# Kernel optimization log

Hardware: AMD Instinct MI355X
Metric: run time of the kernel (lower is better)

The kernel has to match this reference:

```python
import jax, jax.numpy as jnp
import numpy as np

N = 100000
E = 1600000
IN_CH = 128
HID = 64      # hidden_channels, heads=1 -> out_ch per head = 64
OUT = 40      # final classes, heads=1, concat=False -> mean over 1 head
SLOPE = 0.2   # leaky relu slope


def setup_inputs() -> dict:
    key = jax.random.key(0)
    k = jax.random.split(key, 6)
    x = jax.random.normal(k[0], (N, IN_CH), dtype=jnp.float32)
    edge_index = jax.random.randint(k[1], (2, E), 0, N, dtype=jnp.int32)
    # xavier-ish scales
    W0 = jax.random.normal(k[2], (HID, IN_CH), dtype=jnp.float32) * (2.0 / (HID + IN_CH)) ** 0.5
    att0 = jax.random.normal(k[3], (1, 1, 2 * HID), dtype=jnp.float32) * 0.1
    W1 = jax.random.normal(k[4], (OUT, HID), dtype=jnp.float32) * (2.0 / (OUT + HID)) ** 0.5
    att1 = jax.random.normal(k[5], (1, 1, 2 * OUT), dtype=jnp.float32) * 0.1
    return {"x": x, "edge_index": edge_index, "W0": W0, "att0": att0, "W1": W1, "att1": att1}


def _gat_conv(h_in, src, dst, W, att, out_ch, concat):
    # h_in: (N, in_ch) -> h: (N, 1, out_ch)   (heads = 1)
    h = (h_in @ W.T).reshape(N, 1, out_ch)
    x_i = h[dst]                                   # (Etot, 1, out_ch) target feats
    x_j = h[src]                                   # (Etot, 1, out_ch) source feats
    logits = jnp.sum(jnp.concatenate([x_i, x_j], axis=-1) * att, axis=-1)  # (Etot, 1)
    logits = jax.nn.leaky_relu(logits, negative_slope=SLOPE)
    # segment softmax over destination node
    m = jax.ops.segment_max(logits, dst, num_segments=N)
    e = jnp.exp(logits - m[dst])
    s = jax.ops.segment_sum(e, dst, num_segments=N)
    alpha = e / s[dst]                             # (Etot, 1)
    out = jax.ops.segment_sum(x_j * alpha[..., None], dst, num_segments=N)  # (N, 1, out_ch)
    return out.reshape(N, out_ch) if concat else out.mean(axis=1)


def reference(x, edge_index, W0, att0, W1, att1):
    # add_self_loops (applied inside each GATConv with the same node count)
    loops = jnp.arange(N, dtype=edge_index.dtype)
    ei = jnp.concatenate([edge_index, jnp.stack([loops, loops])], axis=1)
    src, dst = ei[0], ei[1]  # PyG source_to_target: x_j = x[src], x_i = x[dst]
    h = _gat_conv(x, src, dst, W0, att0, HID, concat=True)
    h = jax.nn.relu(h)  # dropout inactive in eval mode
    h = _gat_conv(h, src, dst, W1, att1, OUT, concat=False)
    return jax.nn.log_softmax(h, axis=1)
```

## Files before the change

### kernel.cpp

```cpp
#include <hip/hip_runtime.h>
#include <math.h>

#define NNODES 100000
#define NEDGES 1600000
#define ETOT   (NEDGES + NNODES)

#define BSZ   128
#define KBUCK ((NNODES + BSZ - 1) / BSZ)
#define CAP   2816
#define NSUB  8
#define CAPS  768
#define CPAD  16

#define GEMMB 1563
#define EPT   4
#define BUCKB ((ETOT + 1024 - 1) / 1024)
#define GGRP  ((GEMMB + 7) / 8)
#define BGRP  ((BUCKB + 7) / 8)

__device__ __forceinline__ int xcc_id() {
    int x;
    asm volatile("s_getreg_b32 %0, hwreg(HW_REG_XCC_ID)" : "=s"(x));
    return x & (NSUB - 1);
}

__device__ __forceinline__ unsigned short f2bf(float f) {
    unsigned u = __float_as_uint(f);
    return (unsigned short)((u + 0x7FFFu + ((u >> 16) & 1u)) >> 16);
}

__global__ void zero_cnt(int* __restrict__ cnt) {
    int i = blockIdx.x * blockDim.x + threadIdx.x;
    if (i < KBUCK * NSUB * CPAD) cnt[i] = 0;
}

__device__ __forceinline__ void bucket_body(int bb, const int* __restrict__ ei,
                                            int* __restrict__ cnt,
                                            unsigned int* __restrict__ stage) {
    const int t = threadIdx.x;
    const int xg = xcc_id();
#pragma unroll
    for (int r = 0; r < EPT; ++r) {
        int e = bb * 1024 + r * 256 + t;
        if (e < ETOT) {
            int src, dst;
            if (e < NEDGES) { src = ei[e]; dst = ei[NEDGES + e]; }
            else            { src = dst = e - NEDGES; }
            int sb = (dst >> 7) * NSUB + xg;
            int pos = atomicAdd(&cnt[sb * CPAD], 1);
            if (pos < CAPS)
                stage[(size_t)sb * CAPS + pos] =
                    ((unsigned)(dst & 127) << 24) | (unsigned)src;
        }
    }
}

__device__ __forceinline__ void gemm0_body(int gb, const float* __restrict__ x,
                                           const float* __restrict__ W,
                                           const float* __restrict__ att,
                                           unsigned short* __restrict__ h0b,
                                           float* __restrict__ ai,
                                           float* __restrict__ aj) {
    __shared__ float Wt[64 * 68];
    const int tid = threadIdx.x;
    const int nb = gb * 64;

    const int lane = tid & 63;
    const int w    = tid >> 6;
    const int ocg  = lane & 15;
    const int ng   = lane >> 4;
    const int nodeLocal = w * 16 + ng * 4;

    const float* xp[4];
#pragma unroll
    for (int j = 0; j < 4; ++j) {
        int node = nb + nodeLocal + j;
        xp[j] = x + (size_t)(node < NNODES ? node : NNODES - 1) * 128;
    }

    float4 acc[4];
#pragma unroll
    for (int j = 0; j < 4; ++j) acc[j] = make_float4(0.f, 0.f, 0.f, 0.f);

#pragma unroll
    for (int h = 0; h < 2; ++h) {
        if (h) __syncthreads();
        for (int i = tid; i < 64 * 64; i += 256) {
            int oc = i >> 6, k = i & 63;
            Wt[k * 68 + oc] = W[oc * 128 + h * 64 + k];
        }
        __syncthreads();

#pragma unroll 4
        for (int k4 = 0; k4 < 16; ++k4) {
            const int kb = k4 * 4;
            float4 wv0 = *(const float4*)&Wt[(kb + 0) * 68 + ocg * 4];
            float4 wv1 = *(const float4*)&Wt[(kb + 1) * 68 + ocg * 4];
            float4 wv2 = *(const float4*)&Wt[(kb + 2) * 68 + ocg * 4];
            float4 wv3 = *(const float4*)&Wt[(kb + 3) * 68 + ocg * 4];
#pragma unroll
            for (int j = 0; j < 4; ++j) {
                float4 xv = *(const float4*)(xp[j] + h * 64 + kb);
                acc[j].x += xv.x * wv0.x + xv.y * wv1.x + xv.z * wv2.x + xv.w * wv3.x;
                acc[j].y += xv.x * wv0.y + xv.y * wv1.y + xv.z * wv2.y + xv.w * wv3.y;
                acc[j].z += xv.x * wv0.z + xv.y * wv1.z + xv.z * wv2.z + xv.w * wv3.z;
                acc[j].w += xv.x * wv0.w + xv.y * wv1.w + xv.z * wv2.w + xv.w * wv3.w;
            }
        }
    }

    const int ocb = ocg * 4;
    float ati[4], atj[4];
#pragma unroll
    for (int i = 0; i < 4; ++i) {
        ati[i] = att[ocb + i];
        atj[i] = att[64 + ocb + i];
    }

#pragma unroll
    for (int j = 0; j < 4; ++j) {
        int nodeG = nb + nodeLocal + j;
        float pai = acc[j].x * ati[0] + acc[j].y * ati[1] + acc[j].z * ati[2] + acc[j].w * ati[3];
        float paj = acc[j].x * atj[0] + acc[j].y * atj[1] + acc[j].z * atj[2] + acc[j].w * atj[3];
#pragma unroll
        for (int off = 1; off < 16; off <<= 1) {
            pai += __shfl_xor(pai, off, 64);
            paj += __shfl_xor(paj, off, 64);
        }
        if (nodeG < NNODES) {
            unsigned p0 = ((unsigned)f2bf(acc[j].y) << 16) | f2bf(acc[j].x);
            unsigned p1 = ((unsigned)f2bf(acc[j].w) << 16) | f2bf(acc[j].z);
            *(uint2*)&h0b[(size_t)nodeG * 64 + ocb] = make_uint2(p0, p1);
            if (ocg == 0) { ai[nodeG] = pai; aj[nodeG] = paj; }
        }
    }
}

__global__ __launch_bounds__(256) void fusedA(
        const int* __restrict__ ei, int* __restrict__ cnt,
        unsigned int* __restrict__ stage,
        const float* __restrict__ x, const float* __restrict__ W0,
        const float* __restrict__ att0,
        unsigned short* __restrict__ h0b, float* __restrict__ ai0,
        float* __restrict__ aj0) {
    const int bid = blockIdx.x;
    const int grp = bid >> 3, sub = bid & 7;
    if ((grp & 1) && (grp >> 1) < GGRP) {
        int g = (grp >> 1) * 8 + sub;
        if (g < GEMMB) gemm0_body(g, x, W0, att0, h0b, ai0, aj0);
    } else {
        int bg = grp - min(GGRP, (grp + 1) >> 1);
        int bb = bg * 8 + sub;
        if (bb < BUCKB) bucket_body(bb, ei, cnt, stage);
    }
}

__global__ void bucket_scan(const int* __restrict__ cnt, int* __restrict__ bstart) {
    __shared__ int wsum[16];
    const int t = threadIdx.x;
    int x = 0;
    if (t < KBUCK) {
#pragma unroll
        for (int s = 0; s < NSUB; ++s) x += min(cnt[(t * NSUB + s) * CPAD], CAPS);
    }
    int lane = t & 63, w = t >> 6;
    int inc = x;
#pragma unroll
    for (int off = 1; off < 64; off <<= 1) {
        int u = __shfl_up(inc, off, 64);
        if (lane >= off) inc += u;
    }
    if (lane == 63) wsum[w] = inc;
    __syncthreads();
    if (t == 0) {
        int s = 0;
#pragma unroll
        for (int j = 0; j < 16; ++j) { int y = wsum[j]; wsum[j] = s; s += y; }
    }
    __syncthreads();
    int excl = inc - x + wsum[w];
    if (t < KBUCK) bstart[t] = excl;
    if (t == KBUCK) bstart[KBUCK] = excl;
}

__global__ __launch_bounds__(256) void bucket_scatter(
        const int* __restrict__ cnt, const int* __restrict__ bstart,
        const unsigned int* __restrict__ stage, int* __restrict__ rowstart,
        int* __restrict__ csr_src) {
    __shared__ unsigned int ent[CAP];
    __shared__ int hist[BSZ];
    __shared__ int scnt[NSUB];
    __shared__ int soff[NSUB + 1];
    __shared__ int wtot;
    const int b = blockIdx.x, t = threadIdx.x;
    const int n0 = b * BSZ;
    const int base = bstart[b];

    if (t < BSZ) hist[t] = 0;
    if (t < NSUB) scnt[t] = min(cnt[(b * NSUB + t) * CPAD], CAPS);
    __syncthreads();
    if (t == 0) {
        int s = 0;
#pragma unroll
        for (int x = 0; x < NSUB; ++x) { soff[x] = s; s += scnt[x]; }
        soff[NSUB] = s;
    }
    __syncthreads();

#pragma unroll
    for (int x = 0; x < NSUB; ++x) {
        const int cx = scnt[x];
        const int ox = soff[x];
        const unsigned int* sp = stage + (size_t)(b * NSUB + x) * CAPS;
        for (int i = t; i < cx; i += 256) {
            unsigned int v = sp[i];
            ent[ox + i] = v;
            atomicAdd(&hist[v >> 24], 1);
        }
    }
    __syncthreads();
    const int c = soff[NSUB];

    int lane = t & 63, w = t >> 6;
    int v = (t < BSZ) ? hist[t] : 0;
    int inc = v;
#pragma unroll
    for (int off = 1; off < 64; off <<= 1) {
        int u = __shfl_up(inc, off, 64);
        if (lane >= off) inc += u;
    }
    if (t == 63) wtot = inc;
    __syncthreads();
    int excl = inc - v + ((w == 1) ? wtot : 0);
    if (t < BSZ) {
        int node = n0 + t;
        if (node <= NNODES) rowstart[node] = base + excl;
    }
    __syncthreads();
    if (t < BSZ) hist[t] = excl;
    __syncthreads();
    for (int i = t; i < c; i += 256) {
        unsigned int e = ent[i];
        int pos = atomicAdd(&hist[e >> 24], 1);
        csr_src[base + pos] = (int)(e & 0xFFFFFFu);
    }
}

__global__ __launch_bounds__(256) void agg_gemm1(
        const int* __restrict__ rowstart, const int* __restrict__ csr_src,
        const float* __restrict__ aj,
        const float* __restrict__ ai, const unsigned short* __restrict__ h0b,
        const float* __restrict__ W1, const float* __restrict__ att1,
        unsigned short* __restrict__ h1b, float* __restrict__ ai1,
        float* __restrict__ aj1) {
    __shared__ float  W1L[64 * 68];
    __shared__ int2   escr[4][64];
    __shared__ float  rowbuf[4][64];

    const int tid = threadIdx.x;
    for (int i = tid; i < 64 * 64; i += 256) {
        int oc = i >> 6, k = i & 63;
        W1L[oc * 68 + k] = (oc < 40) ? W1[oc * 64 + k] : 0.0f;
    }
    __syncthreads();

    const int lane = tid & 63;
    const int wid  = tid >> 6;
    const int n = blockIdx.x * 4 + wid;
    if (n >= NNODES) return;

    const int start = rowstart[n];
    const int end   = rowstart[n + 1];
    const float ain = ai[n];

    const int cg = lane & 7;
    const int sg = lane >> 3;
    float4 accA = make_float4(0.f, 0.f, 0.f, 0.f);
    float4 accB = make_float4(0.f, 0.f, 0.f, 0.f);
    float  esum = 0.0f;

    for (int c = start; c < end; c += 64) {
        int rem = end - c;
        int cnt = (rem < 64) ? rem : 64;
        int s = 0; float e = 0.0f;
        if (lane < cnt) {
            s = csr_src[c + lane];
            float t = ain + aj[s];
            t = (t > 0.0f) ? t : 0.2f * t;
            e = __expf(t);
        }
        escr[wid][lane] = make_int2(s, __float_as_int(e));
        esum += e;
        for (int j0 = 0; j0 < cnt; j0 += 8) {
            int j = j0 + sg;
            if (j < cnt) {
                int2 v = escr[wid][j];
                float a = __int_as_float(v.y);
                uint4 hv = *(const uint4*)&h0b[(size_t)v.x * 64 + cg * 8];
                float c0 = __uint_as_float(hv.x << 16);
                float c1 = __uint_as_float(hv.x & 0xFFFF0000u);
                float c2 = __uint_as_float(hv.y << 16);
                float c3 = __uint_as_float(hv.y & 0xFFFF0000u);
                float c4 = __uint_as_float(hv.z << 16);
                float c5 = __uint_as_float(hv.z & 0xFFFF0000u);
                float c6 = __uint_as_float(hv.w << 16);
                float c7 = __uint_as_float(hv.w & 0xFFFF0000u);
                accA.x = fmaf(a, c0, accA.x);
                accA.y = fmaf(a, c1, accA.y);
                accA.z = fmaf(a, c2, accA.z);
                accA.w = fmaf(a, c3, accA.w);
                accB.x = fmaf(a, c4, accB.x);
                accB.y = fmaf(a, c5, accB.y);
                accB.z = fmaf(a, c6, accB.z);
                accB.w = fmaf(a, c7, accB.w);
            }
        }
    }
#pragma unroll
    for (int off = 32; off > 0; off >>= 1) esum += __shfl_xor(esum, off, 64);
    const float inv = 1.0f / esum;
#pragma unroll
    for (int off = 8; off < 64; off <<= 1) {
        accA.x += __shfl_xor(accA.x, off, 64);
        accA.y += __shfl_xor(accA.y, off, 64);
        accA.z += __shfl_xor(accA.z, off, 64);
        accA.w += __shfl_xor(accA.w, off, 64);
        accB.x += __shfl_xor(accB.x, off, 64);
        accB.y += __shfl_xor(accB.y, off, 64);
        accB.z += __shfl_xor(accB.z, off, 64);
        accB.w += __shfl_xor(accB.w, off, 64);
    }
    if (sg == 0) {
        float4 rA, rB;
        rA.x = fmaxf(accA.x * inv, 0.0f);
        rA.y = fmaxf(accA.y * inv, 0.0f);
        rA.z = fmaxf(accA.z * inv, 0.0f);
        rA.w = fmaxf(accA.w * inv, 0.0f);
        rB.x = fmaxf(accB.x * inv, 0.0f);
        rB.y = fmaxf(accB.y * inv, 0.0f);
        rB.z = fmaxf(accB.z * inv, 0.0f);
        rB.w = fmaxf(accB.w * inv, 0.0f);
        *(float4*)&rowbuf[wid][cg * 8]     = rA;
        *(float4*)&rowbuf[wid][cg * 8 + 4] = rB;
    }

    const int oc = lane;
    float hacc = 0.0f;
#pragma unroll
    for (int k4 = 0; k4 < 16; ++k4) {
        float4 rv = *(const float4*)&rowbuf[wid][k4 * 4];
        float4 wv = *(const float4*)&W1L[oc * 68 + k4 * 4];
        hacc = fmaf(rv.x, wv.x, hacc);
        hacc = fmaf(rv.y, wv.y, hacc);
        hacc = fmaf(rv.z, wv.z, hacc);
        hacc = fmaf(rv.w, wv.w, hacc);
    }

    const bool ocOK = (oc < 40);
    if (ocOK) h1b[(size_t)n * 40 + oc] = f2bf(hacc);
    float pai = ocOK ? hacc * att1[oc]      : 0.0f;
    float paj = ocOK ? hacc * att1[40 + oc] : 0.0f;
#pragma unroll
    for (int off = 1; off < 64; off <<= 1) {
        pai += __shfl_xor(pai, off, 64);
        paj += __shfl_xor(paj, off, 64);
    }
    if (lane == 0) { ai1[n] = pai; aj1[n] = paj; }
}

__global__ __launch_bounds__(256) void agg_lsm(
        const int* __restrict__ rowstart, const int* __restrict__ csr_src,
        const float* __restrict__ aj,
        const float* __restrict__ ai, const unsigned short* __restrict__ h1b,
        float* __restrict__ out) {
    __shared__ int2 escr[4][64];

    const int lane = threadIdx.x & 63;
    const int wid  = threadIdx.x >> 6;
    const int n = blockIdx.x * 4 + wid;
    if (n >= NNODES) return;

    const int start = rowstart[n];
    const int end   = rowstart[n + 1];
    const float ain = ai[n];

    const int  cg   = lane & 7;
    const int  sg   = lane >> 3;
    const bool chOK = (cg < 5);
    float4 accA = make_float4(0.f, 0.f, 0.f, 0.f);
    float4 accB = make_float4(0.f, 0.f, 0.f, 0.f);
    float  esum = 0.0f;

    for (int c = start; c < end; c += 64) {
        int rem = end - c;
        int cnt = (rem < 64) ? rem : 64;
        int s = 0; float e = 0.0f;
        if (lane < cnt) {
            s = csr_src[c + lane];
            float t = ain + aj[s];
            t = (t > 0.0f) ? t : 0.2f * t;
            e = __expf(t);
        }
        escr[wid][lane] = make_int2(s, __float_as_int(e));
        esum += e;
        for (int j0 = 0; j0 < cnt; j0 += 8) {
            int j = j0 + sg;
            if (chOK && j < cnt) {
                int2 v = escr[wid][j];
                float a = __int_as_float(v.y);
                uint4 hv = *(const uint4*)&h1b[(size_t)v.x * 40 + cg * 8];
                float c0 = __uint_as_float(hv.x << 16);
                float c1 = __uint_as_float(hv.x & 0xFFFF0000u);
                float c2 = __uint_as_float(hv.y << 16);
                float c3 = __uint_as_float(hv.y & 0xFFFF0000u);
                float c4 = __uint_as_float(hv.z << 16);
                float c5 = __uint_as_float(hv.z & 0xFFFF0000u);
                float c6 = __uint_as_float(hv.w << 16);
                float c7 = __uint_as_float(hv.w & 0xFFFF0000u);
                accA.x = fmaf(a, c0, accA.x);
                accA.y = fmaf(a, c1, accA.y);
                accA.z = fmaf(a, c2, accA.z);
                accA.w = fmaf(a, c3, accA.w);
                accB.x = fmaf(a, c4, accB.x);
                accB.y = fmaf(a, c5, accB.y);
                accB.z = fmaf(a, c6, accB.z);
                accB.w = fmaf(a, c7, accB.w);
            }
        }
    }
#pragma unroll
    for (int off = 32; off > 0; off >>= 1) esum += __shfl_xor(esum, off, 64);
    const float inv = 1.0f / esum;
#pragma unroll
    for (int off = 8; off < 64; off <<= 1) {
        accA.x += __shfl_xor(accA.x, off, 64);
        accA.y += __shfl_xor(accA.y, off, 64);
        accA.z += __shfl_xor(accA.z, off, 64);
        accA.w += __shfl_xor(accA.w, off, 64);
        accB.x += __shfl_xor(accB.x, off, 64);
        accB.y += __shfl_xor(accB.y, off, 64);
        accB.z += __shfl_xor(accB.z, off, 64);
        accB.w += __shfl_xor(accB.w, off, 64);
    }
    accA.x *= inv; accA.y *= inv; accA.z *= inv; accA.w *= inv;
    accB.x *= inv; accB.y *= inv; accB.z *= inv; accB.w *= inv;

    float mx = -INFINITY;
    if (chOK) {
        mx = fmaxf(fmaxf(fmaxf(accA.x, accA.y), fmaxf(accA.z, accA.w)),
                   fmaxf(fmaxf(accB.x, accB.y), fmaxf(accB.z, accB.w)));
    }
#pragma unroll
    for (int off = 1; off < 8; off <<= 1) mx = fmaxf(mx, __shfl_xor(mx, off, 64));
    float sm = 0.0f;
    if (chOK) {
        sm = __expf(accA.x - mx) + __expf(accA.y - mx) +
             __expf(accA.z - mx) + __expf(accA.w - mx) +
             __expf(accB.x - mx) + __expf(accB.y - mx) +
             __expf(accB.z - mx) + __expf(accB.w - mx);
    }
#pragma unroll
    for (int off = 1; off < 8; off <<= 1) sm += __shfl_xor(sm, off, 64);
    float ls = mx + logf(sm);
    if (sg == 0 && chOK) {
        float4 oA = make_float4(accA.x - ls, accA.y - ls, accA.z - ls, accA.w - ls);
        float4 oB = make_float4(accB.x - ls, accB.y - ls, accB.z - ls, accB.w - ls);
        *(float4*)&out[(size_t)n * 40 + cg * 8]     = oA;
        *(float4*)&out[(size_t)n * 40 + cg * 8 + 4] = oB;
    }
}

extern "C" void kernel_launch(void* const* d_in, const int* in_sizes, int n_in,
                              void* d_out, int out_size, void* d_ws, size_t ws_size,
                              hipStream_t stream) {
    const float* x    = (const float*)d_in[0];
    const int*   ei   = (const int*)  d_in[1];
    const float* W0   = (const float*)d_in[2];
    const float* att0 = (const float*)d_in[3];
    const float* W1   = (const float*)d_in[4];
    const float* att1 = (const float*)d_in[5];
    float* out = (float*)d_out;

    int* wi = (int*)d_ws;
    int*  cnt      = wi;
    int*  bstart   = cnt + 100352;
    int*  rowstart = bstart + 1024;
    unsigned int* stage = (unsigned int*)(rowstart + 100352);
    int*  csr_src  = (int*)(stage + (size_t)KBUCK * NSUB * CAPS);
    unsigned short* h0b = (unsigned short*)(csr_src + 1700096);
    unsigned short* h1b = h0b + (size_t)NNODES * 64;
    float* fbase = (float*)(h1b + (size_t)NNODES * 40);
    float* ai0 = fbase;
    float* aj0 = ai0 + 100352;
    float* ai1 = aj0 + 100352;
    float* aj1 = ai1 + 100352;

    const int B = 256;
    const int aggGrid = (NNODES + 3) / 4;
    const int fusedGrid = (GGRP + BGRP) * 8;

    zero_cnt<<<(KBUCK * NSUB * CPAD + B - 1) / B, B, 0, stream>>>(cnt);
    fusedA<<<fusedGrid, B, 0, stream>>>(ei, cnt, stage, x, W0, att0, h0b, ai0, aj0);
    bucket_scan<<<1, 1024, 0, stream>>>(cnt, bstart);
    bucket_scatter<<<KBUCK, B, 0, stream>>>(cnt, bstart, stage, rowstart, csr_src);

    agg_gemm1<<<aggGrid, B, 0, stream>>>(rowstart, csr_src, aj0, ai0, h0b,
                                         W1, att1, h1b, ai1, aj1);

    agg_lsm<<<aggGrid, B, 0, stream>>>(rowstart, csr_src, aj1, ai1, h1b, out);
}
```

Measured before the change: 385.9 us.

## Split fused bucket/GEMM kernel and register-prefetch x rows in GEMM0

Replaces the interleaved fused kernel, which mixed edge-bucketing blocks and layer-0 GEMM blocks, with two separate launches. The GEMM now stages the full 128x64 weight matrix in LDS in one pass instead of two halves. It also software-pipelines the x-row loads through a three-deep register queue to hide global latency. The split gives up the concurrency between the atomic-heavy bucketing and the GEMM, and the larger LDS footprint may reduce occupancy.

After: 404.1 us. +4.7%, slower.

```diff
diff --git a/kernel.cpp b/kernel.cpp
--- a/kernel.cpp
+++ b/kernel.cpp
@@ -15,8 +15,6 @@
 #define GEMMB 1563
 #define EPT   4
 #define BUCKB ((ETOT + 1024 - 1) / 1024)
-#define GGRP  ((GEMMB + 7) / 8)
-#define BGRP  ((BUCKB + 7) / 8)
 
 __device__ __forceinline__ int xcc_id() {
     int x;
@@ -34,9 +32,10 @@
     if (i < KBUCK * NSUB * CPAD) cnt[i] = 0;
 }
 
-__device__ __forceinline__ void bucket_body(int bb, const int* __restrict__ ei,
-                                            int* __restrict__ cnt,
-                                            unsigned int* __restrict__ stage) {
+__global__ __launch_bounds__(256) void bucket_build(
+        const int* __restrict__ ei, int* __restrict__ cnt,
+        unsigned int* __restrict__ stage) {
+    const int bb = blockIdx.x;
     const int t = threadIdx.x;
     const int xg = xcc_id();
 #pragma unroll
@@ -55,15 +54,14 @@
     }
 }
 
-__device__ __forceinline__ void gemm0_body(int gb, const float* __restrict__ x,
-                                           const float* __restrict__ W,
-                                           const float* __restrict__ att,
-                                           unsigned short* __restrict__ h0b,
-                                           float* __restrict__ ai,
-                                           float* __restrict__ aj) {
-    __shared__ float Wt[64 * 68];
+__global__ __launch_bounds__(256) void gemm0_k(
+        const float* __restrict__ x, const float* __restrict__ W,
+        const float* __restrict__ att,
+        unsigned short* __restrict__ h0b,
+        float* __restrict__ ai, float* __restrict__ aj) {
+    __shared__ float Wt[128 * 68];
     const int tid = threadIdx.x;
-    const int nb = gb * 64;
+    const int nb = blockIdx.x * 64;
 
     const int lane = tid & 63;
     const int w    = tid >> 6;
@@ -78,35 +76,47 @@
         xp[j] = x + (size_t)(node < NNODES ? node : NNODES - 1) * 128;
     }
 
+    float4 xa[4], xb[4], xc[4];
+#pragma unroll
+    for (int j = 0; j < 4; ++j) {
+        xa[j] = *(const float4*)(xp[j] + 0);
+        xb[j] = *(const float4*)(xp[j] + 4);
+        xc[j] = *(const float4*)(xp[j] + 8);
+    }
+
+    for (int i = tid; i < 128 * 64; i += 256) {
+        int oc = i >> 7, k = i & 127;
+        Wt[k * 68 + oc] = W[i];
+    }
+    __syncthreads();
+
     float4 acc[4];
 #pragma unroll
     for (int j = 0; j < 4; ++j) acc[j] = make_float4(0.f, 0.f, 0.f, 0.f);
 
-#pragma unroll
-    for (int h = 0; h < 2; ++h) {
-        if (h) __syncthreads();
-        for (int i = tid; i < 64 * 64; i += 256) {
-            int oc = i >> 6, k = i & 63;
-            Wt[k * 68 + oc] = W[oc * 128 + h * 64 + k];
-        }
-        __syncthreads();
-
 #pragma unroll 4
-        for (int k4 = 0; k4 < 16; ++k4) {
-            const int kb = k4 * 4;
-            float4 wv0 = *(const float4*)&Wt[(kb + 0) * 68 + ocg * 4];
-            float4 wv1 = *(const float4*)&Wt[(kb + 1) * 68 + ocg * 4];
-            float4 wv2 = *(const float4*)&Wt[(kb + 2) * 68 + ocg * 4];
-            float4 wv3 = *(const float4*)&Wt[(kb + 3) * 68 + ocg * 4];
-#pragma unroll
-            for (int j = 0; j < 4; ++j) {
-                float4 xv = *(const float4*)(xp[j] + h * 64 + kb);
-                acc[j].x += xv.x * wv0.x + xv.y * wv1.x + xv.z * wv2.x + xv.w * wv3.x;
-                acc[j].y += xv.x * wv0.y + xv.y * wv1.y + xv.z * wv2.y + xv.w * wv3.y;
-                acc[j].z += xv.x * wv0.z + xv.y * wv1.z + xv.z * wv2.z + xv.w * wv3.z;
-                acc[j].w += xv.x * wv0.w + xv.y * wv1.w + xv.z * wv2.w + xv.w * wv3.w;
-            }
-        }
+    for (int k4 = 0; k4 < 32; ++k4) {
+        const int kb = k4 * 4;
+        int kpf = kb + 12; if (kpf > 124) kpf = 124;
+        float4 xn0 = *(const float4*)(xp[0] + kpf);
+        float4 xn1 = *(const float4*)(xp[1] + kpf);
+        float4 xn2 = *(const float4*)(xp[2] + kpf);
+        float4 xn3 = *(const float4*)(xp[3] + kpf);
+        float4 wv0 = *(const float4*)&Wt[(kb + 0) * 68 + ocg * 4];
+        float4 wv1 = *(const float4*)&Wt[(kb + 1) * 68 + ocg * 4];
+        float4 wv2 = *(const float4*)&Wt[(kb + 2) * 68 + ocg * 4];
+        float4 wv3 = *(const float4*)&Wt[(kb + 3) * 68 + ocg * 4];
+#pragma unroll
+        for (int j = 0; j < 4; ++j) {
+            float4 xv = xa[j];
+            acc[j].x += xv.x * wv0.x + xv.y * wv1.x + xv.z * wv2.x + xv.w * wv3.x;
+            acc[j].y += xv.x * wv0.y + xv.y * wv1.y + xv.z * wv2.y + xv.w * wv3.y;
+            acc[j].z += xv.x * wv0.z + xv.y * wv1.z + xv.z * wv2.z + xv.w * wv3.z;
+            acc[j].w += xv.x * wv0.w + xv.y * wv1.w + xv.z * wv2.w + xv.w * wv3.w;
+        }
+        xa[0] = xb[0]; xa[1] = xb[1]; xa[2] = xb[2]; xa[3] = xb[3];
+        xb[0] = xc[0]; xb[1] = xc[1]; xb[2] = xc[2]; xb[3] = xc[3];
+        xc[0] = xn0;   xc[1] = xn1;   xc[2] = xn2;   xc[3] = xn3;
     }
 
     const int ocb = ocg * 4;
@@ -133,25 +143,6 @@
             *(uint2*)&h0b[(size_t)nodeG * 64 + ocb] = make_uint2(p0, p1);
             if (ocg == 0) { ai[nodeG] = pai; aj[nodeG] = paj; }
         }
-    }
-}
-
-__global__ __launch_bounds__(256) void fusedA(
-        const int* __restrict__ ei, int* __restrict__ cnt,
-        unsigned int* __restrict__ stage,
-        const float* __restrict__ x, const float* __restrict__ W0,
-        const float* __restrict__ att0,
-        unsigned short* __restrict__ h0b, float* __restrict__ ai0,
-        float* __restrict__ aj0) {
-    const int bid = blockIdx.x;
-    const int grp = bid >> 3, sub = bid & 7;
-    if ((grp & 1) && (grp >> 1) < GGRP) {
-        int g = (grp >> 1) * 8 + sub;
-        if (g < GEMMB) gemm0_body(g, x, W0, att0, h0b, ai0, aj0);
-    } else {
-        int bg = grp - min(GGRP, (grp + 1) >> 1);
-        int bb = bg * 8 + sub;
-        if (bb < BUCKB) bucket_body(bb, ei, cnt, stage);
     }
 }
 
@@ -497,10 +488,10 @@
 
     const int B = 256;
     const int aggGrid = (NNODES + 3) / 4;
-    const int fusedGrid = (GGRP + BGRP) * 8;
 
     zero_cnt<<<(KBUCK * NSUB * CPAD + B - 1) / B, B, 0, stream>>>(cnt);
-    fusedA<<<fusedGrid, B, 0, stream>>>(ei, cnt, stage, x, W0, att0, h0b, ai0, aj0);
+    bucket_build<<<BUCKB, B, 0, stream>>>(ei, cnt, stage);
+    gemm0_k<<<GEMMB, B, 0, stream>>>(x, W0, att0, h0b, ai0, aj0);
     bucket_scan<<<1, 1024, 0, stream>>>(cnt, bstart);
     bucket_scatter<<<KBUCK, B, 0, stream>>>(cnt, bstart, stage, rowstart, csr_src);
 
```

## Stage full W0 in LDS with x prefetch; compute edge weights per-lane via shuffles

Applied to the files above, without the earlier changes.

The layer-0 GEMM now loads all 128 columns of W0 into shared memory in one pass. It also keeps a three-deep register pipeline of x loads so global reads overlap the FMAs, in place of two LDS phases with direct loads. Both aggregation kernels drop the LDS edge scratch buffer. Each lane-group broadcasts the source index with a shuffle and recomputes the attention weight itself, so the sum is scaled by 8 to correct for the repeated computation. This trades redundant aj loads and exp calls (8x duplication) for removing the LDS write/read round trip. The larger LDS footprint may reduce occupancy of the GEMM kernel.

Result: no change. 378.5 us (-1.9%).

```diff
diff --git a/kernel.cpp b/kernel.cpp
--- a/kernel.cpp
+++ b/kernel.cpp
@@ -61,7 +61,7 @@
                                            unsigned short* __restrict__ h0b,
                                            float* __restrict__ ai,
                                            float* __restrict__ aj) {
-    __shared__ float Wt[64 * 68];
+    __shared__ float Wt[128 * 68];
     const int tid = threadIdx.x;
     const int nb = gb * 64;
 
@@ -78,35 +78,47 @@
         xp[j] = x + (size_t)(node < NNODES ? node : NNODES - 1) * 128;
     }
 
+    float4 xa[4], xb[4], xc[4];
+#pragma unroll
+    for (int j = 0; j < 4; ++j) {
+        xa[j] = *(const float4*)(xp[j] + 0);
+        xb[j] = *(const float4*)(xp[j] + 4);
+        xc[j] = *(const float4*)(xp[j] + 8);
+    }
+
+    for (int i = tid; i < 128 * 64; i += 256) {
+        int oc = i >> 7, k = i & 127;
+        Wt[k * 68 + oc] = W[i];
+    }
+    __syncthreads();
+
     float4 acc[4];
 #pragma unroll
     for (int j = 0; j < 4; ++j) acc[j] = make_float4(0.f, 0.f, 0.f, 0.f);
 
-#pragma unroll
-    for (int h = 0; h < 2; ++h) {
-        if (h) __syncthreads();
-        for (int i = tid; i < 64 * 64; i += 256) {
-            int oc = i >> 6, k = i & 63;
-            Wt[k * 68 + oc] = W[oc * 128 + h * 64 + k];
-        }
-        __syncthreads();
-
 #pragma unroll 4
-        for (int k4 = 0; k4 < 16; ++k4) {
-            const int kb = k4 * 4;
-            float4 wv0 = *(const float4*)&Wt[(kb + 0) * 68 + ocg * 4];
-            float4 wv1 = *(const float4*)&Wt[(kb + 1) * 68 + ocg * 4];
-            float4 wv2 = *(const float4*)&Wt[(kb + 2) * 68 + ocg * 4];
-            float4 wv3 = *(const float4*)&Wt[(kb + 3) * 68 + ocg * 4];
-#pragma unroll
-            for (int j = 0; j < 4; ++j) {
-                float4 xv = *(const float4*)(xp[j] + h * 64 + kb);
-                acc[j].x += xv.x * wv0.x + xv.y * wv1.x + xv.z * wv2.x + xv.w * wv3.x;
-                acc[j].y += xv.x * wv0.y + xv.y * wv1.y + xv.z * wv2.y + xv.w * wv3.y;
-                acc[j].z += xv.x * wv0.z + xv.y * wv1.z + xv.z * wv2.z + xv.w * wv3.z;
-                acc[j].w += xv.x * wv0.w + xv.y * wv1.w + xv.z * wv2.w + xv.w * wv3.w;
-            }
-        }
+    for (int k4 = 0; k4 < 32; ++k4) {
+        const int kb = k4 * 4;
+        int kpf = kb + 12; if (kpf > 124) kpf = 124;
+        float4 xn0 = *(const float4*)(xp[0] + kpf);
+        float4 xn1 = *(const float4*)(xp[1] + kpf);
+        float4 xn2 = *(const float4*)(xp[2] + kpf);
+        float4 xn3 = *(const float4*)(xp[3] + kpf);
+        float4 wv0 = *(const float4*)&Wt[(kb + 0) * 68 + ocg * 4];
+        float4 wv1 = *(const float4*)&Wt[(kb + 1) * 68 + ocg * 4];
+        float4 wv2 = *(const float4*)&Wt[(kb + 2) * 68 + ocg * 4];
+        float4 wv3 = *(const float4*)&Wt[(kb + 3) * 68 + ocg * 4];
+#pragma unroll
+        for (int j = 0; j < 4; ++j) {
+            float4 xv = xa[j];
+            acc[j].x += xv.x * wv0.x + xv.y * wv1.x + xv.z * wv2.x + xv.w * wv3.x;
+            acc[j].y += xv.x * wv0.y + xv.y * wv1.y + xv.z * wv2.y + xv.w * wv3.y;
+            acc[j].z += xv.x * wv0.z + xv.y * wv1.z + xv.z * wv2.z + xv.w * wv3.z;
+            acc[j].w += xv.x * wv0.w + xv.y * wv1.w + xv.z * wv2.w + xv.w * wv3.w;
+        }
+        xa[0] = xb[0]; xa[1] = xb[1]; xa[2] = xb[2]; xa[3] = xb[3];
+        xb[0] = xc[0]; xb[1] = xc[1]; xb[2] = xc[2]; xb[3] = xc[3];
+        xc[0] = xn0;   xc[1] = xn1;   xc[2] = xn2;   xc[3] = xn3;
     }
 
     const int ocb = ocg * 4;
@@ -254,7 +266,6 @@
         unsigned short* __restrict__ h1b, float* __restrict__ ai1,
         float* __restrict__ aj1) {
     __shared__ float  W1L[64 * 68];
-    __shared__ int2   escr[4][64];
     __shared__ float  rowbuf[4][64];
 
     const int tid = threadIdx.x;
@@ -275,6 +286,7 @@
 
     const int cg = lane & 7;
     const int sg = lane >> 3;
+    const int cgo = cg << 3;
     float4 accA = make_float4(0.f, 0.f, 0.f, 0.f);
     float4 accB = make_float4(0.f, 0.f, 0.f, 0.f);
     float  esum = 0.0f;
@@ -282,21 +294,17 @@
     for (int c = start; c < end; c += 64) {
         int rem = end - c;
         int cnt = (rem < 64) ? rem : 64;
-        int s = 0; float e = 0.0f;
-        if (lane < cnt) {
-            s = csr_src[c + lane];
-            float t = ain + aj[s];
-            t = (t > 0.0f) ? t : 0.2f * t;
-            e = __expf(t);
-        }
-        escr[wid][lane] = make_int2(s, __float_as_int(e));
-        esum += e;
+        int s = (lane < cnt) ? csr_src[c + lane] : 0;
         for (int j0 = 0; j0 < cnt; j0 += 8) {
-            int j = j0 + sg;
+            int j  = j0 + sg;
+            int sj = __shfl(s, j, 64);
             if (j < cnt) {
-                int2 v = escr[wid][j];
-                float a = __int_as_float(v.y);
-                uint4 hv = *(const uint4*)&h0b[(size_t)v.x * 64 + cg * 8];
+                float ajv = aj[sj];
+                uint4 hv = *(const uint4*)&h0b[(unsigned)(sj << 6) + cgo];
+                float t = ain + ajv;
+                t = (t > 0.0f) ? t : 0.2f * t;
+                float a = __expf(t);
+                esum += a;
                 float c0 = __uint_as_float(hv.x << 16);
                 float c1 = __uint_as_float(hv.x & 0xFFFF0000u);
                 float c2 = __uint_as_float(hv.y << 16);
@@ -318,7 +326,7 @@
     }
 #pragma unroll
     for (int off = 32; off > 0; off >>= 1) esum += __shfl_xor(esum, off, 64);
-    const float inv = 1.0f / esum;
+    const float inv = 8.0f / esum;
 #pragma unroll
     for (int off = 8; off < 64; off <<= 1) {
         accA.x += __shfl_xor(accA.x, off, 64);
@@ -340,8 +348,8 @@
         rB.y = fmaxf(accB.y * inv, 0.0f);
         rB.z = fmaxf(accB.z * inv, 0.0f);
         rB.w = fmaxf(accB.w * inv, 0.0f);
-        *(float4*)&rowbuf[wid][cg * 8]     = rA;
-        *(float4*)&rowbuf[wid][cg * 8 + 4] = rB;
+        *(float4*)&rowbuf[wid][cgo]     = rA;
+        *(float4*)&rowbuf[wid][cgo + 4] = rB;
     }
 
     const int oc = lane;
@@ -373,8 +381,6 @@
         const float* __restrict__ aj,
         const float* __restrict__ ai, const unsigned short* __restrict__ h1b,
         float* __restrict__ out) {
-    __shared__ int2 escr[4][64];
-
     const int lane = threadIdx.x & 63;
     const int wid  = threadIdx.x >> 6;
     const int n = blockIdx.x * 4 + wid;
@@ -394,43 +400,41 @@
     for (int c = start; c < end; c += 64) {
         int rem = end - c;
         int cnt = (rem < 64) ? rem : 64;
-        int s = 0; float e = 0.0f;
-        if (lane < cnt) {
-            s = csr_src[c + lane];
-            float t = ain + aj[s];
-            t = (t > 0.0f) ? t : 0.2f * t;
-            e = __expf(t);
-        }
-        escr[wid][lane] = make_int2(s, __float_as_int(e));
-        esum += e;
+        int s = (lane < cnt) ? csr_src[c + lane] : 0;
         for (int j0 = 0; j0 < cnt; j0 += 8) {
-            int j = j0 + sg;
-            if (chOK && j < cnt) {
-                int2 v = escr[wid][j];
-                float a = __int_as_float(v.y);
-                uint4 hv = *(const uint4*)&h1b[(size_t)v.x * 40 + cg * 8];
-                float c0 = __uint_as_float(hv.x << 16);
-                float c1 = __uint_as_float(hv.x & 0xFFFF0000u);
-                float c2 = __uint_as_float(hv.y << 16);
-                float c3 = __uint_as_float(hv.y & 0xFFFF0000u);
-                float c4 = __uint_as_float(hv.z << 16);
-                float c5 = __uint_as_float(hv.z & 0xFFFF0000u);
-                float c6 = __uint_as_float(hv.w << 16);
-                float c7 = __uint_as_float(hv.w & 0xFFFF0000u);
-                accA.x = fmaf(a, c0, accA.x);
-                accA.y = fmaf(a, c1, accA.y);
-                accA.z = fmaf(a, c2, accA.z);
-                accA.w = fmaf(a, c3, accA.w);
-                accB.x = fmaf(a, c4, accB.x);
-                accB.y = fmaf(a, c5, accB.y);
-                accB.z = fmaf(a, c6, accB.z);
-                accB.w = fmaf(a, c7, accB.w);
+            int j  = j0 + sg;
+            int sj = __shfl(s, j, 64);
+            if (j < cnt) {
+                float ajv = aj[sj];
+                float t = ain + ajv;
+                t = (t > 0.0f) ? t : 0.2f * t;
+                float a = __expf(t);
+                esum += a;
+                if (chOK) {
+                    uint4 hv = *(const uint4*)&h1b[(unsigned)(sj * 40) + (cg << 3)];
+                    float c0 = __uint_as_float(hv.x << 16);
+                    float c1 = __uint_as_float(hv.x & 0xFFFF0000u);
+                    float c2 = __uint_as_float(hv.y << 16);
+                    float c3 = __uint_as_float(hv.y & 0xFFFF0000u);
+                    float c4 = __uint_as_float(hv.z << 16);
+                    float c5 = __uint_as_float(hv.z & 0xFFFF0000u);
+                    float c6 = __uint_as_float(hv.w << 16);
+                    float c7 = __uint_as_float(hv.w & 0xFFFF0000u);
+                    accA.x = fmaf(a, c0, accA.x);
+                    accA.y = fmaf(a, c1, accA.y);
+                    accA.z = fmaf(a, c2, accA.z);
+                    accA.w = fmaf(a, c3, accA.w);
+                    accB.x = fmaf(a, c4, accB.x);
+                    accB.y = fmaf(a, c5, accB.y);
+                    accB.z = fmaf(a, c6, accB.z);
+                    accB.w = fmaf(a, c7, accB.w);
+                }
             }
         }
     }
 #pragma unroll
     for (int off = 32; off > 0; off >>= 1) esum += __shfl_xor(esum, off, 64);
-    const float inv = 1.0f / esum;
+    const float inv = 8.0f / esum;
 #pragma unroll
     for (int off = 8; off < 64; off <<= 1) {
         accA.x += __shfl_xor(accA.x, off, 64);
@@ -465,8 +469,8 @@
     if (sg == 0 && chOK) {
         float4 oA = make_float4(accA.x - ls, accA.y - ls, accA.z - ls, accA.w - ls);
         float4 oB = make_float4(accB.x - ls, accB.y - ls, accB.z - ls, accB.w - ls);
-        *(float4*)&out[(size_t)n * 40 + cg * 8]     = oA;
-        *(float4*)&out[(size_t)n * 40 + cg * 8 + 4] = oB;
+        *(float4*)&out[(size_t)n * 40 + (cg << 3)]     = oA;
+        *(float4*)&out[(size_t)n * 40 + (cg << 3) + 4] = oB;
     }
 }
 
```
